# Performance work log

Measured on AMD Instinct MI355X. Metric: run time of the kernel, lower is better.

Reference implementation:

```python
import jax, jax.numpy as jnp
import numpy as np

D_MODEL = 1024
NUM_HEADS = 16
D_K = D_MODEL // NUM_HEADS
THETA = 10000.0
SEQ = 2048
BATCH = 2


def _rope(t, positions):
    # t: [b, h, s, d_k]; positions: [s]
    half = D_K // 2
    freqs = 1.0 / (THETA ** (jnp.arange(0, D_K, 2, dtype=jnp.float32) / D_K))  # [half]
    angles = positions.astype(jnp.float32)[:, None] * freqs[None, :]  # [s, half]
    cos = jnp.cos(angles)  # [s, half]
    sin = jnp.sin(angles)
    tr = t.reshape(t.shape[:-1] + (half, 2))  # pairs are (even, odd) interleaved
    x1, x2 = tr[..., 0], tr[..., 1]
    r1 = x1 * cos - x2 * sin
    r2 = x1 * sin + x2 * cos
    return jnp.stack([r1, r2], axis=-1).reshape(t.shape)


def setup_inputs() -> dict:
    key = jax.random.key(0)
    ks = jax.random.split(key, 5)
    std = float(np.sqrt(2.0 / (D_MODEL + D_MODEL)))
    return {
        "x": jax.random.normal(ks[0], (BATCH, SEQ, D_MODEL), dtype=jnp.float32),
        "token_positions": jnp.arange(SEQ, dtype=jnp.int64 if jax.config.jax_enable_x64 else jnp.int32),
        "wq": std * jax.random.normal(ks[1], (D_MODEL, D_MODEL), dtype=jnp.float32),
        "wk": std * jax.random.normal(ks[2], (D_MODEL, D_MODEL), dtype=jnp.float32),
        "wv": std * jax.random.normal(ks[3], (D_MODEL, D_MODEL), dtype=jnp.float32),
        "wo": std * jax.random.normal(ks[4], (D_MODEL, D_MODEL), dtype=jnp.float32),
    }


def reference(x, token_positions, wq, wk, wv, wo):
    b, s, _ = x.shape
    # projections: weight is (d_out, d_in), y = x @ W^T
    def proj(w):
        y = jnp.einsum('bsd,od->bso', x, w)
        return y.reshape(b, s, NUM_HEADS, D_K).transpose(0, 2, 1, 3)  # [b,h,s,dk]
    Q, K, V = proj(wq), proj(wk), proj(wv)
    Q = _rope(Q, token_positions)
    K = _rope(K, token_positions)
    scale = 1.0 / jnp.sqrt(jnp.asarray(D_K, dtype=x.dtype))
    scores = jnp.einsum('bhqd,bhkd->bhqk', Q, K) * scale  # [b,h,s,s]
    causal = jnp.tril(jnp.ones((s, s), dtype=bool))
    scores = jnp.where(causal, scores, jnp.asarray(-jnp.inf, dtype=scores.dtype))
    attn = jax.nn.softmax(scores, axis=-1)
    out = jnp.einsum('bhqk,bhkd->bhqd', attn, V)  # [b,h,s,dk]
    out = out.transpose(0, 2, 1, 3).reshape(b, s, D_MODEL)
    return jnp.einsum('bsd,od->bso', out, wo)
```

## Files before the change

kernel.cpp:

```cpp
#include <hip/hip_runtime.h>
#include <hip/hip_bf16.h>
#include <math.h>

#define BATCH  2
#define SEQ    2048
#define DMODEL 1024
#define NHEADS 16
#define DK     64

typedef __hip_bfloat16 bf16;
typedef short s16x8 __attribute__((ext_vector_type(8)));
typedef float f32x4 __attribute__((ext_vector_type(4)));

union P8 { int4 i4; s16x8 v; short s[8]; };

static __device__ __forceinline__ unsigned short f2bu(float f) {
    bf16 h = __float2bfloat16(f);
    return *reinterpret_cast<unsigned short*>(&h);
}

static __device__ __forceinline__ void gll16(const void* g, void* l) {
    __builtin_amdgcn_global_load_lds(
        (const __attribute__((address_space(1))) unsigned int*)g,
        (__attribute__((address_space(3))) unsigned int*)l, 16, 0, 0);
}

__global__ __launch_bounds__(256) void conv_k(
    const float* __restrict__ x, const float* __restrict__ wq,
    const float* __restrict__ wk, const float* __restrict__ wv,
    const float* __restrict__ wo, bf16* __restrict__ dst)
{
    const size_t e0 = ((size_t)blockIdx.x * 256 + threadIdx.x) << 3;
    const float* src;
    bf16* d;
    if (e0 < (size_t)4194304) { src = x + e0; d = dst + e0; }
    else {
        const size_t r = e0 - 4194304;
        const int wsel = (int)(r >> 20);
        const size_t off = r & 1048575;
        src = (wsel == 0 ? wq : wsel == 1 ? wk : wsel == 2 ? wv : wo) + off;
        d = dst + 4194304 + ((size_t)wsel << 20) + off;
    }
    const float4 a = *(const float4*)src;
    const float4 b = *(const float4*)(src + 4);
    P8 p;
    p.s[0] = (short)f2bu(a.x); p.s[1] = (short)f2bu(a.y);
    p.s[2] = (short)f2bu(a.z); p.s[3] = (short)f2bu(a.w);
    p.s[4] = (short)f2bu(b.x); p.s[5] = (short)f2bu(b.y);
    p.s[6] = (short)f2bu(b.z); p.s[7] = (short)f2bu(b.w);
    *(int4*)d = p.i4;
}

__global__ __launch_bounds__(256) void gemm_qkv(
    const bf16* __restrict__ Ab, const bf16* __restrict__ Wb,
    bf16* __restrict__ O0, bf16* __restrict__ O1, bf16* __restrict__ O2)
{
    __shared__ __align__(16) short As[128 * 64];
    __shared__ __align__(16) short Ws[128 * 64];
    const int tid  = threadIdx.x;
    const int w    = tid >> 6;
    const int lane = tid & 63;
    const int ln   = lane & 15;
    const int quad = lane >> 4;
    const int id   = blockIdx.x;
    const int m_base = (id & 31) << 7;
    const int n_base = ((id >> 5) & 7) << 7;
    const int z = id >> 8;
    const bf16* Wz = Wb + ((size_t)z << 20);

    const int lrw = lane >> 3;
    const int lcs = ((lane & 7) ^ lrw) << 3;
    const size_t abase = (size_t)(m_base + 32 * w + lrw) * DMODEL + lcs;
    const size_t wbase = (size_t)(n_base + 32 * w + lrw) * DMODEL + lcs;
    short* ldsA = &As[2048 * w];
    short* ldsW = &Ws[2048 * w];

    const f32x4 zero4 = {0.f, 0.f, 0.f, 0.f};
    f32x4 acc[4][4];
    #pragma unroll
    for (int i = 0; i < 4; ++i)
        #pragma unroll
        for (int j = 0; j < 4; ++j) acc[i][j] = zero4;

    const int mo = (w >> 1) << 6, no = (w & 1) << 6;
    const int swz = ln & 7;

    for (int k0 = 0; k0 < DMODEL; k0 += 64) {
        __syncthreads();
        #pragma unroll
        for (int t = 0; t < 4; ++t) {
            gll16(Ab + abase + (size_t)t * 8 * DMODEL + k0, ldsA + t * 512);
            gll16(Wz + wbase + (size_t)t * 8 * DMODEL + k0, ldsW + t * 512);
        }
        __syncthreads();
        #pragma unroll
        for (int t = 0; t < 2; ++t) {
            const int co = (((t << 2) + quad) ^ swz) << 3;
            s16x8 af[4], bw[4];
            #pragma unroll
            for (int i = 0; i < 4; ++i) {
                af[i] = *(const s16x8*)&As[(mo + 16 * i + ln) * 64 + co];
                bw[i] = *(const s16x8*)&Ws[(no + 16 * i + ln) * 64 + co];
            }
            #pragma unroll
            for (int mi = 0; mi < 4; ++mi)
                #pragma unroll
                for (int ni = 0; ni < 4; ++ni)
                    acc[mi][ni] = __builtin_amdgcn_mfma_f32_16x16x32_bf16(
                        af[mi], bw[ni], acc[mi][ni], 0, 0, 0);
        }
    }

    if (z < 2) {
        bf16* C = (z == 0) ? O0 : O1;
        const float qs = (z == 0) ? 0.125f : 1.0f;
        const int h = (n_base + no) >> 6;
        const float sgn = (ln & 1) ? 1.0f : -1.0f;
        float freq[4];
        #pragma unroll
        for (int ni = 0; ni < 4; ++ni)
            freq[ni] = exp2f(-(float)((16 * ni + ln) >> 1) * 0.4152410119f);
        #pragma unroll
        for (int mi = 0; mi < 4; ++mi) {
            #pragma unroll
            for (int r = 0; r < 4; ++r) {
                const int m = m_base + mo + 16 * mi + quad * 4 + r;
                const int b = m >> 11, s = m & (SEQ - 1);
                const float fs = (float)s;
                float sn[4], cs[4];
                #pragma unroll
                for (int ni = 0; ni < 4; ++ni)
                    __sincosf(fs * freq[ni], &sn[ni], &cs[ni]);
                bf16* row = C + (((size_t)(b * NHEADS + h) * SEQ) + s) * DK;
                #pragma unroll
                for (int ni = 0; ni < 4; ++ni) {
                    const float v = acc[mi][ni][r];
                    const float p = __shfl_xor(v, 1, 64);
                    row[16 * ni + ln] =
                        __float2bfloat16((v * cs[ni] + sgn * p * sn[ni]) * qs);
                }
            }
        }
    } else {
        #pragma unroll
        for (int ni = 0; ni < 4; ++ni) {
            const int n = n_base + no + 16 * ni + ln;
            const int h = n >> 6, d = n & (DK - 1);
            #pragma unroll
            for (int mi = 0; mi < 4; ++mi) {
                const int m0v = m_base + mo + 16 * mi + quad * 4;
                const int b = m0v >> 11, s0 = m0v & (SEQ - 1);
                ushort4 pk;
                pk.x = f2bu(acc[mi][ni][0]); pk.y = f2bu(acc[mi][ni][1]);
                pk.z = f2bu(acc[mi][ni][2]); pk.w = f2bu(acc[mi][ni][3]);
                *(ushort4*)(O2 + (((size_t)(b * NHEADS + h) * DK) + d) * SEQ + s0) = pk;
            }
        }
    }
}

__global__ __launch_bounds__(256) void gemm_wo(
    const bf16* __restrict__ Ab, const bf16* __restrict__ Wb,
    float* __restrict__ Of)
{
    __shared__ __align__(16) short As[64 * 64];
    __shared__ __align__(16) short Ws[128 * 64];
    const int tid  = threadIdx.x;
    const int w    = tid >> 6;
    const int lane = tid & 63;
    const int ln   = lane & 15;
    const int quad = lane >> 4;
    const int id   = blockIdx.x;
    const int m_base = (id & 63) << 6;
    const int n_base = (id >> 6) << 7;

    const int lrw = lane >> 3;
    const int lcs = ((lane & 7) ^ lrw) << 3;
    const int am = m_base + 16 * w + lrw;
    short* ldsA = &As[1024 * w];
    const size_t wbase = (size_t)(n_base + 32 * w + lrw) * DMODEL + lcs;
    short* ldsW = &Ws[2048 * w];

    const f32x4 zero4 = {0.f, 0.f, 0.f, 0.f};
    f32x4 acc[2][4];
    #pragma unroll
    for (int i = 0; i < 2; ++i)
        #pragma unroll
        for (int j = 0; j < 4; ++j) acc[i][j] = zero4;

    const int mo = (w >> 1) << 5, no = (w & 1) << 6;
    const int swz = ln & 7;

    for (int k0 = 0; k0 < DMODEL; k0 += 64) {
        const int hh = k0 >> 6;
        __syncthreads();
        #pragma unroll
        for (int t = 0; t < 2; ++t) {
            const int m = am + t * 8;
            const int b = m >> 11, s = m & (SEQ - 1);
            gll16(Ab + (((size_t)(b * NHEADS + hh) * SEQ) + s) * DK + lcs,
                  ldsA + t * 512);
        }
        #pragma unroll
        for (int t = 0; t < 4; ++t)
            gll16(Wb + wbase + (size_t)t * 8 * DMODEL + k0, ldsW + t * 512);
        __syncthreads();
        #pragma unroll
        for (int t = 0; t < 2; ++t) {
            const int co = (((t << 2) + quad) ^ swz) << 3;
            s16x8 af[2], bw[4];
            #pragma unroll
            for (int i = 0; i < 2; ++i)
                af[i] = *(const s16x8*)&As[(mo + 16 * i + ln) * 64 + co];
            #pragma unroll
            for (int j = 0; j < 4; ++j)
                bw[j] = *(const s16x8*)&Ws[(no + 16 * j + ln) * 64 + co];
            #pragma unroll
            for (int mi = 0; mi < 2; ++mi)
                #pragma unroll
                for (int ni = 0; ni < 4; ++ni)
                    acc[mi][ni] = __builtin_amdgcn_mfma_f32_16x16x32_bf16(
                        af[mi], bw[ni], acc[mi][ni], 0, 0, 0);
        }
    }

    #pragma unroll
    for (int mi = 0; mi < 2; ++mi)
        #pragma unroll
        for (int ni = 0; ni < 4; ++ni) {
            const int n = n_base + no + 16 * ni + ln;
            #pragma unroll
            for (int r = 0; r < 4; ++r) {
                const int m = m_base + mo + 16 * mi + quad * 4 + r;
                Of[(size_t)m * DMODEL + n] = acc[mi][ni][r];
            }
        }
}

__global__ __launch_bounds__(256) void attn_k(bf16* __restrict__ Q,
                                              const bf16* __restrict__ Kg,
                                              const bf16* __restrict__ VT)
{
    __shared__ __align__(16) short Ks[64 * 72];
    __shared__ __align__(16) short Vs[64 * 72];
    __shared__ __align__(16) short PT[64 * 72];
    const int tid  = threadIdx.x;
    const int w    = tid >> 6;
    const int lane = tid & 63;
    const int ln   = lane & 15;
    const int quad = lane >> 4;
    const int bh = blockIdx.x & 31;
    const int qt = 31 - (blockIdx.x >> 5);
    const size_t base = (size_t)bh * (SEQ * DK);
    const int srow = tid >> 2;
    const int sc   = (tid & 3) << 4;
    const int qrow = qt * 64 + 16 * w + ln;

    P8 qa0, qa1;
    {
        const bf16* qsrc = Q + base + (size_t)qrow * DK + quad * 8;
        qa0.i4 = *(const int4*)(qsrc);
        qa1.i4 = *(const int4*)(qsrc + 32);
    }
    const f32x4 zero4 = {0.f, 0.f, 0.f, 0.f};
    f32x4 o[4];
    #pragma unroll
    for (int mt = 0; mt < 4; ++mt) o[mt] = zero4;
    float lsum = 0.f;

    P8 kk[2], vv[2];
    {
        const bf16* ksrc = Kg + base + (size_t)srow * DK + sc;
        kk[0].i4 = *(const int4*)(ksrc);
        kk[1].i4 = *(const int4*)(ksrc + 8);
        const bf16* vsrc = VT + base + (size_t)srow * SEQ + sc;
        vv[0].i4 = *(const int4*)(vsrc);
        vv[1].i4 = *(const int4*)(vsrc + 8);
    }

    for (int kb = 0; kb <= qt; ++kb) {
        __syncthreads();
        *(s16x8*)&Ks[srow * 72 + sc]     = kk[0].v;
        *(s16x8*)&Ks[srow * 72 + sc + 8] = kk[1].v;
        *(s16x8*)&Vs[srow * 72 + sc]     = vv[0].v;
        *(s16x8*)&Vs[srow * 72 + sc + 8] = vv[1].v;
        __syncthreads();

        if (kb < qt) {
            const bf16* ksrc = Kg + base + (size_t)((kb + 1) * 64 + srow) * DK + sc;
            kk[0].i4 = *(const int4*)(ksrc);
            kk[1].i4 = *(const int4*)(ksrc + 8);
            const bf16* vsrc = VT + base + (size_t)srow * SEQ + (kb + 1) * 64 + sc;
            vv[0].i4 = *(const int4*)(vsrc);
            vv[1].i4 = *(const int4*)(vsrc + 8);
        }

        f32x4 sf[4];
        #pragma unroll
        for (int mt = 0; mt < 4; ++mt) {
            sf[mt] = zero4;
            s16x8 ka  = *(const s16x8*)&Ks[(16 * mt + ln) * 72 + quad * 8];
            s16x8 kb2 = *(const s16x8*)&Ks[(16 * mt + ln) * 72 + 32 + quad * 8];
            sf[mt] = __builtin_amdgcn_mfma_f32_16x16x32_bf16(ka,  qa0.v, sf[mt], 0, 0, 0);
            sf[mt] = __builtin_amdgcn_mfma_f32_16x16x32_bf16(kb2, qa1.v, sf[mt], 0, 0, 0);
        }

        if (kb == qt) {
            #pragma unroll
            for (int mt = 0; mt < 4; ++mt)
                #pragma unroll
                for (int r = 0; r < 4; ++r)
                    if (kb * 64 + 16 * mt + quad * 4 + r > qrow) sf[mt][r] = -INFINITY;
        }
        #pragma unroll
        for (int mt = 0; mt < 4; ++mt)
            #pragma unroll
            for (int r = 0; r < 4; ++r) {
                sf[mt][r] = __expf(sf[mt][r]);
                lsum += sf[mt][r];
            }

        #pragma unroll
        for (int mt = 0; mt < 4; ++mt) {
            ushort4 pk;
            pk.x = f2bu(sf[mt][0]); pk.y = f2bu(sf[mt][1]);
            pk.z = f2bu(sf[mt][2]); pk.w = f2bu(sf[mt][3]);
            *(ushort4*)&PT[(16 * w + ln) * 72 + 16 * mt + quad * 4] = pk;
        }

        s16x8 pa0 = *(const s16x8*)&PT[(16 * w + ln) * 72 + quad * 8];
        s16x8 pa1 = *(const s16x8*)&PT[(16 * w + ln) * 72 + 32 + quad * 8];
        #pragma unroll
        for (int mt = 0; mt < 4; ++mt) {
            s16x8 va0 = *(const s16x8*)&Vs[(16 * mt + ln) * 72 + quad * 8];
            s16x8 va1 = *(const s16x8*)&Vs[(16 * mt + ln) * 72 + 32 + quad * 8];
            o[mt] = __builtin_amdgcn_mfma_f32_16x16x32_bf16(va0, pa0, o[mt], 0, 0, 0);
            o[mt] = __builtin_amdgcn_mfma_f32_16x16x32_bf16(va1, pa1, o[mt], 0, 0, 0);
        }
    }

    lsum += __shfl_xor(lsum, 16, 64);
    lsum += __shfl_xor(lsum, 32, 64);
    const float inv = 1.0f / lsum;
    #pragma unroll
    for (int mt = 0; mt < 4; ++mt) {
        ushort4 st;
        st.x = f2bu(o[mt][0] * inv); st.y = f2bu(o[mt][1] * inv);
        st.z = f2bu(o[mt][2] * inv); st.w = f2bu(o[mt][3] * inv);
        *(ushort4*)(Q + base + (size_t)qrow * DK + 16 * mt + quad * 4) = st;
    }
}

extern "C" void kernel_launch(void* const* d_in, const int* in_sizes, int n_in,
                              void* d_out, int out_size, void* d_ws, size_t ws_size,
                              hipStream_t stream)
{
    const float* x  = (const float*)d_in[0];
    const float* wq = (const float*)d_in[2];
    const float* wk = (const float*)d_in[3];
    const float* wv = (const float*)d_in[4];
    const float* wo = (const float*)d_in[5];

    bf16* wsb   = (bf16*)d_ws;
    bf16* xb    = wsb;
    bf16* wqkvb = wsb + ((size_t)4 << 20);
    bf16* wob   = wsb + ((size_t)7 << 20);
    bf16* Qw    = wsb + ((size_t)8 << 20);
    bf16* Kw    = wsb + ((size_t)12 << 20);
    bf16* VTw   = wsb + ((size_t)16 << 20);

    conv_k<<<4096, 256, 0, stream>>>(x, wq, wk, wv, wo, wsb);
    gemm_qkv<<<768, 256, 0, stream>>>(xb, wqkvb, Qw, Kw, VTw);
    attn_k<<<1024, 256, 0, stream>>>(Qw, Kw, VTw);
    gemm_wo<<<512, 256, 0, stream>>>(Qw, wob, (float*)d_out);
}
```

Baseline: 177.5 us.

## Process two query tiles per attention block to reuse K/V loads

Each attention workgroup now handles 128 query rows, as two 64-row halves per wave, instead of 64. Every K/V tile staged in LDS is used by both halves, which halves global K/V traffic and the number of barrier rounds per query row. The grid shrinks from 1024 to 512 blocks, with a reordered tile schedule for load balance. In exchange each block uses more registers and a larger P buffer in LDS, and the last diagonal tile of the first half does wasted masked work.

```diff
diff --git a/kernel.cpp b/kernel.cpp
--- a/kernel.cpp
+++ b/kernel.cpp
@@ -243,30 +243,36 @@
 {
     __shared__ __align__(16) short Ks[64 * 72];
     __shared__ __align__(16) short Vs[64 * 72];
-    __shared__ __align__(16) short PT[64 * 72];
+    __shared__ __align__(16) short PT[128 * 72];
     const int tid  = threadIdx.x;
     const int w    = tid >> 6;
     const int lane = tid & 63;
     const int ln   = lane & 15;
     const int quad = lane >> 4;
-    const int bh = blockIdx.x & 31;
-    const int qt = 31 - (blockIdx.x >> 5);
+    const int id = blockIdx.x;
+    const int bh = id & 31;
+    const int g  = id >> 5;
+    const int Jt = (g < 8) ? (15 - g) : (g - 8);
     const size_t base = (size_t)bh * (SEQ * DK);
     const int srow = tid >> 2;
     const int sc   = (tid & 3) << 4;
-    const int qrow = qt * 64 + 16 * w + ln;
-
-    P8 qa0, qa1;
+    const int q0 = Jt * 128 + 16 * w + ln;
+    const int q1 = q0 + 64;
+
+    P8 qa0, qa1, qb0, qb1;
     {
-        const bf16* qsrc = Q + base + (size_t)qrow * DK + quad * 8;
+        const bf16* qsrc = Q + base + (size_t)q0 * DK + quad * 8;
         qa0.i4 = *(const int4*)(qsrc);
         qa1.i4 = *(const int4*)(qsrc + 32);
+        const bf16* qsrc1 = Q + base + (size_t)q1 * DK + quad * 8;
+        qb0.i4 = *(const int4*)(qsrc1);
+        qb1.i4 = *(const int4*)(qsrc1 + 32);
     }
     const f32x4 zero4 = {0.f, 0.f, 0.f, 0.f};
-    f32x4 o[4];
+    f32x4 oA[4], oB[4];
     #pragma unroll
-    for (int mt = 0; mt < 4; ++mt) o[mt] = zero4;
-    float lsum = 0.f;
+    for (int mt = 0; mt < 4; ++mt) { oA[mt] = zero4; oB[mt] = zero4; }
+    float lsA = 0.f, lsB = 0.f;
 
     P8 kk[2], vv[2];
     {
@@ -278,7 +284,11 @@
         vv[1].i4 = *(const int4*)(vsrc + 8);
     }
 
-    for (int kb = 0; kb <= qt; ++kb) {
+    const int prA = (16 * w + ln) * 72;
+    const int prB = (64 + 16 * w + ln) * 72;
+    const int kmax = 2 * Jt + 1;
+
+    for (int kb = 0; kb <= kmax; ++kb) {
         __syncthreads();
         *(s16x8*)&Ks[srow * 72 + sc]     = kk[0].v;
         *(s16x8*)&Ks[srow * 72 + sc + 8] = kk[1].v;
@@ -286,7 +296,7 @@
         *(s16x8*)&Vs[srow * 72 + sc + 8] = vv[1].v;
         __syncthreads();
 
-        if (kb < qt) {
+        if (kb < kmax) {
             const bf16* ksrc = Kg + base + (size_t)((kb + 1) * 64 + srow) * DK + sc;
             kk[0].i4 = *(const int4*)(ksrc);
             kk[1].i4 = *(const int4*)(ksrc + 8);
@@ -295,59 +305,75 @@
             vv[1].i4 = *(const int4*)(vsrc + 8);
         }
 
-        f32x4 sf[4];
+        f32x4 sfA[4], sfB[4];
         #pragma unroll
         for (int mt = 0; mt < 4; ++mt) {
-            sf[mt] = zero4;
-            s16x8 ka  = *(const s16x8*)&Ks[(16 * mt + ln) * 72 + quad * 8];
-            s16x8 kb2 = *(const s16x8*)&Ks[(16 * mt + ln) * 72 + 32 + quad * 8];
-            sf[mt] = __builtin_amdgcn_mfma_f32_16x16x32_bf16(ka,  qa0.v, sf[mt], 0, 0, 0);
-            sf[mt] = __builtin_amdgcn_mfma_f32_16x16x32_bf16(kb2, qa1.v, sf[mt], 0, 0, 0);
-        }
-
-        if (kb == qt) {
+            s16x8 ka = *(const s16x8*)&Ks[(16 * mt + ln) * 72 + quad * 8];
+            s16x8 kc = *(const s16x8*)&Ks[(16 * mt + ln) * 72 + 32 + quad * 8];
+            sfA[mt] = zero4;
+            sfA[mt] = __builtin_amdgcn_mfma_f32_16x16x32_bf16(ka, qa0.v, sfA[mt], 0, 0, 0);
+            sfA[mt] = __builtin_amdgcn_mfma_f32_16x16x32_bf16(kc, qa1.v, sfA[mt], 0, 0, 0);
+            sfB[mt] = zero4;
+            sfB[mt] = __builtin_amdgcn_mfma_f32_16x16x32_bf16(ka, qb0.v, sfB[mt], 0, 0, 0);
+            sfB[mt] = __builtin_amdgcn_mfma_f32_16x16x32_bf16(kc, qb1.v, sfB[mt], 0, 0, 0);
+        }
+
+        if (kb >= kmax - 1) {
             #pragma unroll
             for (int mt = 0; mt < 4; ++mt)
                 #pragma unroll
-                for (int r = 0; r < 4; ++r)
-                    if (kb * 64 + 16 * mt + quad * 4 + r > qrow) sf[mt][r] = -INFINITY;
-        }
-        #pragma unroll
-        for (int mt = 0; mt < 4; ++mt)
+                for (int r = 0; r < 4; ++r) {
+                    const int key = kb * 64 + 16 * mt + quad * 4 + r;
+                    if (key > q0) sfA[mt][r] = -INFINITY;
+                    if (key > q1) sfB[mt][r] = -INFINITY;
+                }
+        }
+        #pragma unroll
+        for (int mt = 0; mt < 4; ++mt) {
             #pragma unroll
             for (int r = 0; r < 4; ++r) {
-                sf[mt][r] = __expf(sf[mt][r]);
-                lsum += sf[mt][r];
+                sfA[mt][r] = __expf(sfA[mt][r]);  lsA += sfA[mt][r];
+                sfB[mt][r] = __expf(sfB[mt][r]);  lsB += sfB[mt][r];
             }
-
+            ushort4 pa, pb;
+            pa.x = f2bu(sfA[mt][0]); pa.y = f2bu(sfA[mt][1]);
+            pa.z = f2bu(sfA[mt][2]); pa.w = f2bu(sfA[mt][3]);
+            pb.x = f2bu(sfB[mt][0]); pb.y = f2bu(sfB[mt][1]);
+            pb.z = f2bu(sfB[mt][2]); pb.w = f2bu(sfB[mt][3]);
+            *(ushort4*)&PT[prA + 16 * mt + quad * 4] = pa;
+            *(ushort4*)&PT[prB + 16 * mt + quad * 4] = pb;
+        }
+
+        s16x8 paA0 = *(const s16x8*)&PT[prA + quad * 8];
+        s16x8 paA1 = *(const s16x8*)&PT[prA + 32 + quad * 8];
+        s16x8 paB0 = *(const s16x8*)&PT[prB + quad * 8];
+        s16x8 paB1 = *(const s16x8*)&PT[prB + 32 + quad * 8];
         #pragma unroll
         for (int mt = 0; mt < 4; ++mt) {
-            ushort4 pk;
-            pk.x = f2bu(sf[mt][0]); pk.y = f2bu(sf[mt][1]);
-            pk.z = f2bu(sf[mt][2]); pk.w = f2bu(sf[mt][3]);
-            *(ushort4*)&PT[(16 * w + ln) * 72 + 16 * mt + quad * 4] = pk;
-        }
-
-        s16x8 pa0 = *(const s16x8*)&PT[(16 * w + ln) * 72 + quad * 8];
-        s16x8 pa1 = *(const s16x8*)&PT[(16 * w + ln) * 72 + 32 + quad * 8];
-        #pragma unroll
-        for (int mt = 0; mt < 4; ++mt) {
-            s16x8 va0 = *(const s16x8*)&Vs[(16 * mt + ln) * 72 + quad * 8];
-            s16x8 va1 = *(const s16x8*)&Vs[(16 * mt + ln) * 72 + 32 + quad * 8];
-            o[mt] = __builtin_amdgcn_mfma_f32_16x16x32_bf16(va0, pa0, o[mt], 0, 0, 0);
-            o[mt] = __builtin_amdgcn_mfma_f32_16x16x32_bf16(va1, pa1, o[mt], 0, 0, 0);
-        }
-    }
-
-    lsum += __shfl_xor(lsum, 16, 64);
-    lsum += __shfl_xor(lsum, 32, 64);
-    const float inv = 1.0f / lsum;
+            s16x8 va = *(const s16x8*)&Vs[(16 * mt + ln) * 72 + quad * 8];
+            s16x8 vb = *(const s16x8*)&Vs[(16 * mt + ln) * 72 + 32 + quad * 8];
+            oA[mt] = __builtin_amdgcn_mfma_f32_16x16x32_bf16(va, paA0, oA[mt], 0, 0, 0);
+            oA[mt] = __builtin_amdgcn_mfma_f32_16x16x32_bf16(vb, paA1, oA[mt], 0, 0, 0);
+            oB[mt] = __builtin_amdgcn_mfma_f32_16x16x32_bf16(va, paB0, oB[mt], 0, 0, 0);
+            oB[mt] = __builtin_amdgcn_mfma_f32_16x16x32_bf16(vb, paB1, oB[mt], 0, 0, 0);
+        }
+    }
+
+    lsA += __shfl_xor(lsA, 16, 64);
+    lsA += __shfl_xor(lsA, 32, 64);
+    lsB += __shfl_xor(lsB, 16, 64);
+    lsB += __shfl_xor(lsB, 32, 64);
+    const float invA = 1.0f / lsA;
+    const float invB = 1.0f / lsB;
     #pragma unroll
     for (int mt = 0; mt < 4; ++mt) {
-        ushort4 st;
-        st.x = f2bu(o[mt][0] * inv); st.y = f2bu(o[mt][1] * inv);
-        st.z = f2bu(o[mt][2] * inv); st.w = f2bu(o[mt][3] * inv);
-        *(ushort4*)(Q + base + (size_t)qrow * DK + 16 * mt + quad * 4) = st;
+        ushort4 sa, sb;
+        sa.x = f2bu(oA[mt][0] * invA); sa.y = f2bu(oA[mt][1] * invA);
+        sa.z = f2bu(oA[mt][2] * invA); sa.w = f2bu(oA[mt][3] * invA);
+        *(ushort4*)(Q + base + (size_t)q0 * DK + 16 * mt + quad * 4) = sa;
+        sb.x = f2bu(oB[mt][0] * invB); sb.y = f2bu(oB[mt][1] * invB);
+        sb.z = f2bu(oB[mt][2] * invB); sb.w = f2bu(oB[mt][3] * invB);
+        *(ushort4*)(Q + base + (size_t)q1 * DK + 16 * mt + quad * 4) = sb;
     }
 }
 
@@ -371,6 +397,6 @@
 
     conv_k<<<4096, 256, 0, stream>>>(x, wq, wk, wv, wo, wsb);
     gemm_qkv<<<768, 256, 0, stream>>>(xb, wqkvb, Qw, Kw, VTw);
-    attn_k<<<1024, 256, 0, stream>>>(Qw, Kw, VTw);
+    attn_k<<<512, 256, 0, stream>>>(Qw, Kw, VTw);
     gemm_wo<<<512, 256, 0, stream>>>(Qw, wob, (float*)d_out);
 }
```

Measured after the change: 179.4 us. No clear change (+1.1%).
